# Optimization experiments

Measured on AMD Instinct MI355X. Metric: run time of the kernel, lower is better.

Reference implementation:

```python
import jax, jax.numpy as jnp
import numpy as np

N = 50000
E = 400000
IN_DIM = 256
HID = 64
HEADS = 8
OUT_DIM = 40
NEG_SLOPE = 0.2  # PyG GATConv leaky-relu slope


def gat_conv(x, src, dst, W, a_src, a_dst, bias, concat):
    """One PyG-style GATConv (eval mode, self-loops already appended).
    x: [N, in], W: [in, H*C], a_src/a_dst: [H, C], bias: [H*C] or [C]."""
    H, C = a_src.shape
    h = (x @ W).reshape(N, H, C)                       # [N, H, C]
    # per-node attention logits, gathered per edge
    e_src = (h * a_src[None]).sum(-1)                  # [N, H]
    e_dst = (h * a_dst[None]).sum(-1)                  # [N, H]
    alpha = jax.nn.leaky_relu(e_src[src] + e_dst[dst], NEG_SLOPE)  # [Etot, H]
    # segment softmax over incoming edges of each dst node
    amax = jax.ops.segment_max(alpha, dst, num_segments=N)         # [N, H]
    ex = jnp.exp(alpha - amax[dst])
    denom = jax.ops.segment_sum(ex, dst, num_segments=N)           # [N, H]
    coef = ex / denom[dst]                                         # [Etot, H]
    # weighted scatter-add of neighbor features
    msg = h[src] * coef[:, :, None]                                # [Etot, H, C]
    out = jax.ops.segment_sum(msg, dst, num_segments=N)            # [N, H, C]
    out = out.reshape(N, H * C) if concat else out.mean(axis=1)
    return out + bias


def setup_inputs() -> dict:
    key = jax.random.key(0)
    ks = jax.random.split(key, 10)
    x = jax.random.normal(ks[0], (N, IN_DIM), dtype=jnp.float32)
    edge_index = jax.random.randint(ks[1], (2, E), 0, N, dtype=jnp.int32)
    g1 = 1.0 / np.sqrt(IN_DIM)
    g2 = 1.0 / np.sqrt(HID * HEADS)
    W1 = jax.random.normal(ks[2], (IN_DIM, HEADS * HID), dtype=jnp.float32) * g1
    a_src1 = jax.random.normal(ks[3], (HEADS, HID), dtype=jnp.float32) * 0.1
    a_dst1 = jax.random.normal(ks[4], (HEADS, HID), dtype=jnp.float32) * 0.1
    b1 = jnp.zeros((HEADS * HID,), dtype=jnp.float32)
    W2 = jax.random.normal(ks[5], (HEADS * HID, OUT_DIM), dtype=jnp.float32) * g2
    a_src2 = jax.random.normal(ks[6], (1, OUT_DIM), dtype=jnp.float32) * 0.1
    a_dst2 = jax.random.normal(ks[7], (1, OUT_DIM), dtype=jnp.float32) * 0.1
    b2 = jnp.zeros((OUT_DIM,), dtype=jnp.float32)
    return {"x": x, "edge_index": edge_index, "W1": W1, "a_src1": a_src1,
            "a_dst1": a_dst1, "b1": b1, "W2": W2, "a_src2": a_src2,
            "a_dst2": a_dst2, "b2": b2}


def reference(x, edge_index, W1, a_src1, a_dst1, b1, W2, a_src2, a_dst2, b2):
    # append self loops (PyG GATConv default add_self_loops=True)
    loop = jnp.arange(N, dtype=edge_index.dtype)
    src = jnp.concatenate([edge_index[0], loop])
    dst = jnp.concatenate([edge_index[1], loop])
    h = gat_conv(x, src, dst, W1, a_src1, a_dst1, b1, concat=True)
    h = jax.nn.elu(h)
    # dropout is identity in eval mode
    out = gat_conv(h, src, dst, W2, a_src2, a_dst2, b2, concat=False)
    return out
```

## Files before the change

kernel.cpp:

```cpp
#include <hip/hip_runtime.h>
#include <hip/hip_bf16.h>
#include <math.h>

#define IN_DIM 256
#define HEADS 8
#define HID 64
#define HC1 512
#define OUT_DIM 40
#define NEG_SLOPE 0.2f

typedef __attribute__((ext_vector_type(8))) short short8;
typedef __attribute__((ext_vector_type(4))) float f32x4;

__device__ __forceinline__ unsigned short f2b(float f) {
    __hip_bfloat16 h = __float2bfloat16(f);
    unsigned short u;
    __builtin_memcpy(&u, &h, 2);
    return u;
}

#define LRELU(a) ((a) > 0.f ? (a) : NEG_SLOPE * (a))

__global__ __launch_bounds__(256) void prep_weights(
    const float* __restrict__ W1, const float* __restrict__ W2,
    __hip_bfloat16* __restrict__ W1T, __hip_bfloat16* __restrict__ W2T)
{
    int i = blockIdx.x * 256 + threadIdx.x;
    if (i < HC1 * IN_DIM) {
        int n = i >> 8, k = i & 255;
        W1T[i] = __float2bfloat16(W1[(size_t)k * HC1 + n]);
    }
    int j = i - HC1 * IN_DIM;
    if (j >= 0 && j < 48 * HC1) {
        int n = j >> 9, k = j & 511;
        W2T[j] = __float2bfloat16(n < OUT_DIM ? W2[(size_t)k * OUT_DIM + n] : 0.f);
    }
}


__global__ __launch_bounds__(256) void degree_kernel(
    const int* __restrict__ ei, int* __restrict__ deg, int E, int ET)
{
    int e = blockIdx.x * 256 + threadIdx.x;
    if (e >= ET) return;
    int d = (e < E) ? ei[E + e] : e - E;
    atomicAdd(&deg[d], 1);
}

__global__ __launch_bounds__(256) void scan1_kernel(
    const int* __restrict__ deg, int* __restrict__ rowptr,
    int* __restrict__ aux, int N)
{
    __shared__ int sd[256];
    int tid = threadIdx.x;
    int i = blockIdx.x * 256 + tid;
    int v = (i < N) ? deg[i] : 0;
    sd[tid] = v;
    __syncthreads();
    for (int off = 1; off < 256; off <<= 1) {
        int t = (tid >= off) ? sd[tid - off] : 0;
        __syncthreads();
        sd[tid] += t;
        __syncthreads();
    }
    if (i < N) rowptr[i] = sd[tid] - v;
    if (tid == 255) aux[blockIdx.x] = sd[255];
}

__global__ __launch_bounds__(256) void scan_aux_kernel(int* __restrict__ aux, int nb)
{
    __shared__ int sd[256];
    int tid = threadIdx.x;
    int v = (tid < nb) ? aux[tid] : 0;
    sd[tid] = v;
    __syncthreads();
    for (int off = 1; off < 256; off <<= 1) {
        int t = (tid >= off) ? sd[tid - off] : 0;
        __syncthreads();
        sd[tid] += t;
        __syncthreads();
    }
    if (tid < nb) aux[tid] = sd[tid] - v;
}

__global__ __launch_bounds__(256) void scan_add_kernel(
    int* __restrict__ rowptr, const int* __restrict__ aux, int N, int ET)
{
    int i = blockIdx.x * 256 + threadIdx.x;
    if (i < N) rowptr[i] += aux[blockIdx.x];
    if (i == 0) rowptr[N] = ET;
}

__global__ __launch_bounds__(256) void build_kernel(
    const int* __restrict__ ei, int* __restrict__ cursor,
    int* __restrict__ csr_src, int E, int ET)
{
    int e = blockIdx.x * 256 + threadIdx.x;
    if (e >= ET) return;
    int s, d;
    if (e < E) { s = ei[e]; d = ei[E + e]; } else { s = d = e - E; }
    int pos = atomicAdd(&cursor[d], 1);
    csr_src[pos] = s;
}

__global__ __launch_bounds__(512) void gemm1_mfma(
    const float* __restrict__ x, const __hip_bfloat16* __restrict__ W1T,
    const float* __restrict__ a_src1, const float* __restrict__ a_dst1,
    __hip_bfloat16* __restrict__ h1, float* __restrict__ e_src1,
    float* __restrict__ e_dst1, int N)
{
    __shared__ __hip_bfloat16 As[64][264];
    const int tid = threadIdx.x;
    const int row0 = blockIdx.x * 64;

    {
        int rr = tid >> 3;
        int cb = (tid & 7) * 32;
        int rowc = row0 + rr; if (rowc >= N) rowc = N - 1;
        const float* xp = x + (size_t)rowc * IN_DIM + cb;
#pragma unroll
        for (int j = 0; j < 4; ++j) {
            float4 a0 = *(const float4*)(xp + 8 * j);
            float4 a1 = *(const float4*)(xp + 8 * j + 4);
            short8 v;
            v[0] = f2b(a0.x); v[1] = f2b(a0.y); v[2] = f2b(a0.z); v[3] = f2b(a0.w);
            v[4] = f2b(a1.x); v[5] = f2b(a1.y); v[6] = f2b(a1.z); v[7] = f2b(a1.w);
            *(short8*)(&As[rr][cb + 8 * j]) = v;
        }
    }
    __syncthreads();

    const int w = tid >> 6;
    const int lane = tid & 63;
    const int r = lane & 15, g = lane >> 4;

    f32x4 acc[4][4] = {};
    const short* bp = (const short*)W1T + (size_t)(w * 64 + r) * IN_DIM + 8 * g;

#pragma unroll 2
    for (int kk = 0; kk < IN_DIM; kk += 32) {
        short8 af[4];
#pragma unroll
        for (int rt = 0; rt < 4; ++rt)
            af[rt] = *(const short8*)(&As[rt * 16 + r][kk + 8 * g]);
        short8 bf[4];
#pragma unroll
        for (int t = 0; t < 4; ++t)
            bf[t] = *(const short8*)(bp + (size_t)t * 16 * IN_DIM + kk);
#pragma unroll
        for (int t = 0; t < 4; ++t)
#pragma unroll
            for (int rt = 0; rt < 4; ++rt)
                acc[rt][t] = __builtin_amdgcn_mfma_f32_16x16x32_bf16(
                    af[rt], bf[t], acc[rt][t], 0, 0, 0);
    }

#pragma unroll
    for (int rt = 0; rt < 4; ++rt)
#pragma unroll
        for (int t = 0; t < 4; ++t) {
            int c = w * 64 + t * 16 + r;
#pragma unroll
            for (int q = 0; q < 4; ++q) {
                int row = row0 + rt * 16 + 4 * g + q;
                if (row < N)
                    h1[(size_t)row * HC1 + c] = __float2bfloat16(acc[rt][t][q]);
            }
        }

    float a1v[4], a2v[4];
#pragma unroll
    for (int t = 0; t < 4; ++t) {
        a1v[t] = a_src1[w * 64 + t * 16 + r];
        a2v[t] = a_dst1[w * 64 + t * 16 + r];
    }
#pragma unroll
    for (int rt = 0; rt < 4; ++rt) {
        float ps[4] = {}, pd[4] = {};
#pragma unroll
        for (int t = 0; t < 4; ++t)
#pragma unroll
            for (int q = 0; q < 4; ++q) {
                ps[q] += acc[rt][t][q] * a1v[t];
                pd[q] += acc[rt][t][q] * a2v[t];
            }
#pragma unroll
        for (int off = 1; off < 16; off <<= 1)
#pragma unroll
            for (int q = 0; q < 4; ++q) {
                ps[q] += __shfl_xor(ps[q], off);
                pd[q] += __shfl_xor(pd[q], off);
            }
        if (r == 0) {
#pragma unroll
            for (int q = 0; q < 4; ++q) {
                int row = row0 + rt * 16 + 4 * g + q;
                if (row < N) {
                    e_src1[row * 8 + w] = ps[q];
                    e_dst1[row * 8 + w] = pd[q];
                }
            }
        }
    }
}

__global__ __launch_bounds__(256) void gather1_kernel(
    const int* __restrict__ rowptr, const int* __restrict__ csr_src,
    const __hip_bfloat16* __restrict__ h1, const float* __restrict__ e_src,
    const float* __restrict__ e_dst, const float* __restrict__ b1,
    __hip_bfloat16* __restrict__ hmid, int N)
{
    int d = blockIdx.x * 4 + (threadIdx.x >> 6);
    if (d >= N) return;
    const int lane = threadIdx.x & 63;
    const int h0 = lane >> 3;
    const int base = rowptr[d];
    const int deg = rowptr[d + 1] - base;
    const float edv = e_dst[d * 8 + (lane & 7)];

    float acc[8] = {};
    float ssum = 0.f;

    const int nch = (deg + 7) >> 3;
    for (int c = 0; c < nch; ++c) {
        int i = c * 8 + (lane >> 3);
        int ii = i < deg ? i : deg - 1;
        int s = csr_src[base + ii];
        float v = e_src[s * 8 + (lane & 7)] + edv;
        float coef = (i < deg) ? __expf(LRELU(v)) : 0.f;

        int emax = deg - c * 8; if (emax > 8) emax = 8;
        for (int e = 0; e < emax; ++e) {
            float ce = __shfl(coef, e * 8 + h0);
            int se = __shfl(s, e * 8);
            uint4 u = *(const uint4*)(h1 + (size_t)se * HC1 + 8 * lane);
            acc[0] += ce * __uint_as_float(u.x << 16);
            acc[1] += ce * __uint_as_float(u.x & 0xffff0000u);
            acc[2] += ce * __uint_as_float(u.y << 16);
            acc[3] += ce * __uint_as_float(u.y & 0xffff0000u);
            acc[4] += ce * __uint_as_float(u.z << 16);
            acc[5] += ce * __uint_as_float(u.z & 0xffff0000u);
            acc[6] += ce * __uint_as_float(u.w << 16);
            acc[7] += ce * __uint_as_float(u.w & 0xffff0000u);
            ssum += ce;
        }
    }

    float inv = 1.f / ssum;
    float4 b0 = *(const float4*)(b1 + 8 * lane);
    float4 b4 = *(const float4*)(b1 + 8 * lane + 4);
    float ob[8];
    ob[0] = acc[0] * inv + b0.x; ob[1] = acc[1] * inv + b0.y;
    ob[2] = acc[2] * inv + b0.z; ob[3] = acc[3] * inv + b0.w;
    ob[4] = acc[4] * inv + b4.x; ob[5] = acc[5] * inv + b4.y;
    ob[6] = acc[6] * inv + b4.z; ob[7] = acc[7] * inv + b4.w;
    unsigned short rr[8];
#pragma unroll
    for (int j = 0; j < 8; ++j) {
        float o = ob[j];
        o = o > 0.f ? o : expm1f(o);
        rr[j] = f2b(o);
    }
    *(uint4*)(hmid + (size_t)d * HC1 + 8 * lane) = *(uint4*)rr;
}

__global__ __launch_bounds__(256) void gemm2_mfma(
    const __hip_bfloat16* __restrict__ hmid, const __hip_bfloat16* __restrict__ W2T,
    const float* __restrict__ a_src2, const float* __restrict__ a_dst2,
    float* __restrict__ h2, float* __restrict__ e_src2, float* __restrict__ e_dst2,
    int N)
{
    __shared__ __hip_bfloat16 Bs[48][520];
    const int tid = threadIdx.x;

    {
        const short* wp = (const short*)W2T;
#pragma unroll
        for (int i = 0; i < 12; ++i) {
            int idx = tid + i * 256;
            int row = idx >> 6, ch = idx & 63;
            *(short8*)(&Bs[row][ch * 8]) = *(const short8*)(wp + (size_t)row * HC1 + ch * 8);
        }
    }
    __syncthreads();

    const int w = tid >> 6;
    const int lane = tid & 63;
    const int r = lane & 15, g = lane >> 4;
    const int rowW = blockIdx.x * 64 + w * 16;

    int arow = rowW + r; if (arow >= N) arow = N - 1;
    const short* ap = (const short*)hmid + (size_t)arow * HC1 + 8 * g;

    f32x4 acc[3] = {};
#pragma unroll 4
    for (int kk = 0; kk < HC1; kk += 32) {
        short8 af = *(const short8*)(ap + kk);
        short8 bf[3];
#pragma unroll
        for (int t = 0; t < 3; ++t)
            bf[t] = *(const short8*)(&Bs[t * 16 + r][kk + 8 * g]);
#pragma unroll
        for (int t = 0; t < 3; ++t)
            acc[t] = __builtin_amdgcn_mfma_f32_16x16x32_bf16(af, bf[t], acc[t], 0, 0, 0);
    }

#pragma unroll
    for (int t = 0; t < 3; ++t) {
        int c = t * 16 + r;
        if (c < OUT_DIM) {
#pragma unroll
            for (int q = 0; q < 4; ++q) {
                int row = rowW + 4 * g + q;
                if (row < N) h2[(size_t)row * OUT_DIM + c] = acc[t][q];
            }
        }
    }

    float as[3], ad[3];
#pragma unroll
    for (int t = 0; t < 3; ++t) {
        int c = t * 16 + r;
        as[t] = (c < OUT_DIM) ? a_src2[c] : 0.f;
        ad[t] = (c < OUT_DIM) ? a_dst2[c] : 0.f;
    }
    float ps[4] = {}, pd[4] = {};
#pragma unroll
    for (int t = 0; t < 3; ++t)
#pragma unroll
        for (int q = 0; q < 4; ++q) {
            ps[q] += acc[t][q] * as[t];
            pd[q] += acc[t][q] * ad[t];
        }
#pragma unroll
    for (int off = 1; off < 16; off <<= 1)
#pragma unroll
        for (int q = 0; q < 4; ++q) {
            ps[q] += __shfl_xor(ps[q], off);
            pd[q] += __shfl_xor(pd[q], off);
        }
    if (r == 0) {
#pragma unroll
        for (int q = 0; q < 4; ++q) {
            int row = rowW + 4 * g + q;
            if (row < N) { e_src2[row] = ps[q]; e_dst2[row] = pd[q]; }
        }
    }
}

__global__ __launch_bounds__(256) void gather2_kernel(
    const int* __restrict__ rowptr, const int* __restrict__ csr_src,
    const float* __restrict__ h2, const float* __restrict__ e_src,
    const float* __restrict__ e_dst, const float* __restrict__ b2,
    float* __restrict__ out, int N)
{
    int wid = (blockIdx.x * blockDim.x + threadIdx.x) >> 6;
    if (wid >= N) return;
    const int lane = threadIdx.x & 63;
    const int base = rowptr[wid];
    const int deg = rowptr[wid + 1] - base;
    const float edv = e_dst[wid];
    const bool act = lane < OUT_DIM;

    float acc = 0.f, ssum = 0.f;
    for (int c = 0; c < deg; c += 64) {
        int i = c + lane;
        int ii = i < deg ? i : deg - 1;
        int s = csr_src[base + ii];
        float v = e_src[s] + edv;
        float coef = (i < deg) ? __expf(LRELU(v)) : 0.f;

        int emax = deg - c; if (emax > 64) emax = 64;
#pragma unroll 4
        for (int e = 0; e < emax; ++e) {
            float ce = __shfl(coef, e);
            int se = __shfl(s, e);
            if (act) {
                acc += ce * h2[(size_t)se * OUT_DIM + lane];
                ssum += ce;
            }
        }
    }
    if (act)
        out[(size_t)wid * OUT_DIM + lane] = acc / ssum + b2[lane];
}

extern "C" void kernel_launch(void* const* d_in, const int* in_sizes, int n_in,
                              void* d_out, int out_size, void* d_ws, size_t ws_size,
                              hipStream_t stream)
{
    const float* x      = (const float*)d_in[0];
    const int*   ei     = (const int*)d_in[1];
    const float* W1     = (const float*)d_in[2];
    const float* a_src1 = (const float*)d_in[3];
    const float* a_dst1 = (const float*)d_in[4];
    const float* b1     = (const float*)d_in[5];
    const float* W2     = (const float*)d_in[6];
    const float* a_src2 = (const float*)d_in[7];
    const float* a_dst2 = (const float*)d_in[8];
    const float* b2     = (const float*)d_in[9];
    float* out = (float*)d_out;

    const int N  = in_sizes[0] / IN_DIM;
    const int E  = in_sizes[1] / 2;
    const int ET = E + N;

    char* p = (char*)d_ws;
    auto alloc = [&](size_t bytes) -> void* {
        void* r = (void*)p;
        p += (bytes + 255) & ~(size_t)255;
        return r;
    };
    __hip_bfloat16* h1b    = (__hip_bfloat16*)alloc((size_t)N * HC1 * 2);
    __hip_bfloat16* hmid   = (__hip_bfloat16*)alloc((size_t)N * HC1 * 2);
    float*    h2      = (float*)alloc((size_t)N * OUT_DIM * 4);
    float*    e_src1  = (float*)alloc((size_t)N * HEADS * 4);
    float*    e_dst1  = (float*)alloc((size_t)N * HEADS * 4);
    float*    e_src2  = (float*)alloc((size_t)N * 4);
    float*    e_dst2  = (float*)alloc((size_t)N * 4);
    int*      deg     = (int*)alloc((size_t)N * 4);
    int*      rowptr  = (int*)alloc((size_t)(N + 1) * 4);
    int*      cursor  = (int*)alloc((size_t)N * 4);
    int*      csr_src = (int*)alloc((size_t)ET * 4);
    int*      aux     = (int*)alloc(256 * 4);
    __hip_bfloat16* W1T = (__hip_bfloat16*)alloc((size_t)HC1 * IN_DIM * 2);
    __hip_bfloat16* W2T = (__hip_bfloat16*)alloc((size_t)48 * HC1 * 2);

    const int nbN  = (N + 255) / 256;
    const int nbET = (ET + 255) / 256;

    prep_weights<<<(HC1 * IN_DIM + 48 * HC1 + 255) / 256, 256, 0, stream>>>(
        W1, W2, W1T, W2T);

    hipMemsetAsync(deg, 0, (size_t)N * 4, stream);
    degree_kernel<<<nbET, 256, 0, stream>>>(ei, deg, E, ET);
    scan1_kernel<<<nbN, 256, 0, stream>>>(deg, rowptr, aux, N);
    scan_aux_kernel<<<1, 256, 0, stream>>>(aux, nbN);
    scan_add_kernel<<<nbN, 256, 0, stream>>>(rowptr, aux, N, ET);
    hipMemcpyAsync(cursor, rowptr, (size_t)N * 4, hipMemcpyDeviceToDevice, stream);
    build_kernel<<<nbET, 256, 0, stream>>>(ei, cursor, csr_src, E, ET);

    gemm1_mfma<<<(N + 63) / 64, 512, 0, stream>>>(x, W1T, a_src1, a_dst1, h1b,
                                                  e_src1, e_dst1, N);
    gather1_kernel<<<(N + 3) / 4, 256, 0, stream>>>(rowptr, csr_src, h1b, e_src1,
                                                    e_dst1, b1, hmid, N);

    gemm2_mfma<<<(N + 63) / 64, 256, 0, stream>>>(hmid, W2T, a_src2, a_dst2, h2,
                                                  e_src2, e_dst2, N);
    gather2_kernel<<<(N + 3) / 4, 256, 0, stream>>>(rowptr, csr_src, h2, e_src2,
                                                    e_dst2, b2, out, N);
}
```

Before: 246.9 us.

## Fuse prologue launches, batch gather1 loads, and restructure gather2 loop

Merges the weight-conversion and degree-count kernels into one launch and writes the cursor copy inside scan_add, removing a launch and a device memcpy. In gather1 the per-edge loop is split so that all 8 neighbor-row loads are issued before accumulation, raising memory-level parallelism at the cost of wasted loads on partial chunks. gather2 drops the cross-lane shuffle scheme: each lane now reads the edge indices and logits itself and unrolls by 4. This trades redundant scalar loads for fewer shuffles and more loads in flight.

```diff
diff --git a/kernel.cpp b/kernel.cpp
--- a/kernel.cpp
+++ b/kernel.cpp
@@ -21,31 +21,33 @@
 
 #define LRELU(a) ((a) > 0.f ? (a) : NEG_SLOPE * (a))
 
-__global__ __launch_bounds__(256) void prep_weights(
+#define NB_W ((HC1 * IN_DIM + 48 * HC1 + 255) / 256)
+
+__global__ __launch_bounds__(256) void prologue_kernel(
     const float* __restrict__ W1, const float* __restrict__ W2,
-    __hip_bfloat16* __restrict__ W1T, __hip_bfloat16* __restrict__ W2T)
-{
-    int i = blockIdx.x * 256 + threadIdx.x;
-    if (i < HC1 * IN_DIM) {
-        int n = i >> 8, k = i & 255;
-        W1T[i] = __float2bfloat16(W1[(size_t)k * HC1 + n]);
-    }
-    int j = i - HC1 * IN_DIM;
-    if (j >= 0 && j < 48 * HC1) {
-        int n = j >> 9, k = j & 511;
-        W2T[j] = __float2bfloat16(n < OUT_DIM ? W2[(size_t)k * OUT_DIM + n] : 0.f);
-    }
-}
-
-
-__global__ __launch_bounds__(256) void degree_kernel(
+    __hip_bfloat16* __restrict__ W1T, __hip_bfloat16* __restrict__ W2T,
     const int* __restrict__ ei, int* __restrict__ deg, int E, int ET)
 {
-    int e = blockIdx.x * 256 + threadIdx.x;
-    if (e >= ET) return;
-    int d = (e < E) ? ei[E + e] : e - E;
-    atomicAdd(&deg[d], 1);
-}
+    int b = blockIdx.x;
+    if (b < NB_W) {
+        int i = b * 256 + threadIdx.x;
+        if (i < HC1 * IN_DIM) {
+            int n = i >> 8, k = i & 255;
+            W1T[i] = __float2bfloat16(W1[(size_t)k * HC1 + n]);
+        }
+        int j = i - HC1 * IN_DIM;
+        if (j >= 0 && j < 48 * HC1) {
+            int n = j >> 9, k = j & 511;
+            W2T[j] = __float2bfloat16(n < OUT_DIM ? W2[(size_t)k * OUT_DIM + n] : 0.f);
+        }
+    } else {
+        int e = (b - NB_W) * 256 + threadIdx.x;
+        if (e >= ET) return;
+        int d = (e < E) ? ei[E + e] : e - E;
+        atomicAdd(&deg[d], 1);
+    }
+}
+
 
 __global__ __launch_bounds__(256) void scan1_kernel(
     const int* __restrict__ deg, int* __restrict__ rowptr,
@@ -84,10 +86,15 @@
 }
 
 __global__ __launch_bounds__(256) void scan_add_kernel(
-    int* __restrict__ rowptr, const int* __restrict__ aux, int N, int ET)
+    int* __restrict__ rowptr, int* __restrict__ cursor,
+    const int* __restrict__ aux, int N, int ET)
 {
     int i = blockIdx.x * 256 + threadIdx.x;
-    if (i < N) rowptr[i] += aux[blockIdx.x];
+    if (i < N) {
+        int v = rowptr[i] + aux[blockIdx.x];
+        rowptr[i] = v;
+        cursor[i] = v;
+    }
     if (i == 0) rowptr[N] = ET;
 }
 
@@ -229,20 +236,25 @@
         float v = e_src[s * 8 + (lane & 7)] + edv;
         float coef = (i < deg) ? __expf(LRELU(v)) : 0.f;
 
-        int emax = deg - c * 8; if (emax > 8) emax = 8;
-        for (int e = 0; e < emax; ++e) {
-            float ce = __shfl(coef, e * 8 + h0);
+        uint4 u[8];
+        float ce[8];
+#pragma unroll
+        for (int e = 0; e < 8; ++e) {
+            ce[e] = __shfl(coef, e * 8 + h0);
             int se = __shfl(s, e * 8);
-            uint4 u = *(const uint4*)(h1 + (size_t)se * HC1 + 8 * lane);
-            acc[0] += ce * __uint_as_float(u.x << 16);
-            acc[1] += ce * __uint_as_float(u.x & 0xffff0000u);
-            acc[2] += ce * __uint_as_float(u.y << 16);
-            acc[3] += ce * __uint_as_float(u.y & 0xffff0000u);
-            acc[4] += ce * __uint_as_float(u.z << 16);
-            acc[5] += ce * __uint_as_float(u.z & 0xffff0000u);
-            acc[6] += ce * __uint_as_float(u.w << 16);
-            acc[7] += ce * __uint_as_float(u.w & 0xffff0000u);
-            ssum += ce;
+            u[e] = *(const uint4*)(h1 + (size_t)se * HC1 + 8 * lane);
+        }
+#pragma unroll
+        for (int e = 0; e < 8; ++e) {
+            acc[0] += ce[e] * __uint_as_float(u[e].x << 16);
+            acc[1] += ce[e] * __uint_as_float(u[e].x & 0xffff0000u);
+            acc[2] += ce[e] * __uint_as_float(u[e].y << 16);
+            acc[3] += ce[e] * __uint_as_float(u[e].y & 0xffff0000u);
+            acc[4] += ce[e] * __uint_as_float(u[e].z << 16);
+            acc[5] += ce[e] * __uint_as_float(u[e].z & 0xffff0000u);
+            acc[6] += ce[e] * __uint_as_float(u[e].w << 16);
+            acc[7] += ce[e] * __uint_as_float(u[e].w & 0xffff0000u);
+            ssum += ce[e];
         }
     }
 
@@ -356,30 +368,34 @@
 {
     int wid = (blockIdx.x * blockDim.x + threadIdx.x) >> 6;
     if (wid >= N) return;
-    const int lane = threadIdx.x & 63;
-    const int base = rowptr[wid];
-    const int deg = rowptr[wid + 1] - base;
-    const float edv = e_dst[wid];
-    const bool act = lane < OUT_DIM;
+    int lane = threadIdx.x & 63;
+    int base = rowptr[wid], end = rowptr[wid + 1];
+    float ed = e_dst[wid];
+    bool act = lane < OUT_DIM;
+    int ln = act ? lane : 0;
 
     float acc = 0.f, ssum = 0.f;
-    for (int c = 0; c < deg; c += 64) {
-        int i = c + lane;
-        int ii = i < deg ? i : deg - 1;
-        int s = csr_src[base + ii];
-        float v = e_src[s] + edv;
-        float coef = (i < deg) ? __expf(LRELU(v)) : 0.f;
-
-        int emax = deg - c; if (emax > 64) emax = 64;
-#pragma unroll 4
-        for (int e = 0; e < emax; ++e) {
-            float ce = __shfl(coef, e);
-            int se = __shfl(s, e);
-            if (act) {
-                acc += ce * h2[(size_t)se * OUT_DIM + lane];
-                ssum += ce;
-            }
-        }
+    int j = base;
+    for (; j + 4 <= end; j += 4) {
+        int s0 = csr_src[j], s1 = csr_src[j + 1], s2 = csr_src[j + 2], s3 = csr_src[j + 3];
+        float v0 = e_src[s0] + ed, v1 = e_src[s1] + ed;
+        float v2 = e_src[s2] + ed, v3 = e_src[s3] + ed;
+        float f0 = h2[(size_t)s0 * OUT_DIM + ln];
+        float f1 = h2[(size_t)s1 * OUT_DIM + ln];
+        float f2 = h2[(size_t)s2 * OUT_DIM + ln];
+        float f3 = h2[(size_t)s3 * OUT_DIM + ln];
+        float e0 = __expf(LRELU(v0)), e1 = __expf(LRELU(v1));
+        float e2 = __expf(LRELU(v2)), e3 = __expf(LRELU(v3));
+        acc += e0 * f0 + e1 * f1 + e2 * f2 + e3 * f3;
+        ssum += e0 + e1 + e2 + e3;
+    }
+    for (; j < end; ++j) {
+        int s0 = csr_src[j];
+        float v0 = e_src[s0] + ed;
+        float f0 = h2[(size_t)s0 * OUT_DIM + ln];
+        float e0 = __expf(LRELU(v0));
+        acc += e0 * f0;
+        ssum += e0;
     }
     if (act)
         out[(size_t)wid * OUT_DIM + lane] = acc / ssum + b2[lane];
@@ -429,15 +445,12 @@
     const int nbN  = (N + 255) / 256;
     const int nbET = (ET + 255) / 256;
 
-    prep_weights<<<(HC1 * IN_DIM + 48 * HC1 + 255) / 256, 256, 0, stream>>>(
-        W1, W2, W1T, W2T);
-
     hipMemsetAsync(deg, 0, (size_t)N * 4, stream);
-    degree_kernel<<<nbET, 256, 0, stream>>>(ei, deg, E, ET);
+    prologue_kernel<<<NB_W + nbET, 256, 0, stream>>>(W1, W2, W1T, W2T, ei, deg, E, ET);
+
     scan1_kernel<<<nbN, 256, 0, stream>>>(deg, rowptr, aux, N);
     scan_aux_kernel<<<1, 256, 0, stream>>>(aux, nbN);
-    scan_add_kernel<<<nbN, 256, 0, stream>>>(rowptr, aux, N, ET);
-    hipMemcpyAsync(cursor, rowptr, (size_t)N * 4, hipMemcpyDeviceToDevice, stream);
+    scan_add_kernel<<<nbN, 256, 0, stream>>>(rowptr, cursor, aux, N, ET);
     build_kernel<<<nbET, 256, 0, stream>>>(ei, cursor, csr_src, E, ET);
 
     gemm1_mfma<<<(N + 63) / 64, 512, 0, stream>>>(x, W1T, a_src1, a_dst1, h1b,
```

Measured after the change: 235.1 us. -4.8%, faster.
